# Performance work log

Hardware: AMD Instinct MI355X
Metric: run time of the kernel (lower is better)

The kernel has to match this reference:

```python
import jax, jax.numpy as jnp
import numpy as np

B, Q, K, H, DQ, DK, DV = 16, 128, 512, 128, 128, 128, 128
MASK_VALUE = -1000000.0  # matches d2l.sequence_mask fill value


def setup_inputs() -> dict:
    key = jax.random.key(0)
    ks = jax.random.split(key, 7)
    queries = jax.random.normal(ks[0], (B, Q, DQ), dtype=jnp.float32)
    keys = jax.random.normal(ks[1], (B, K, DK), dtype=jnp.float32)
    values = jax.random.normal(ks[2], (B, K, DV), dtype=jnp.float32)
    valid_lens = jax.random.randint(ks[3], (B,), 1, K + 1, dtype=jnp.int32)
    # Linear params (no bias), scaled like torch default init ~ 1/sqrt(fan_in)
    W_q = jax.random.normal(ks[4], (DQ, H), dtype=jnp.float32) / np.sqrt(DQ)
    W_k = jax.random.normal(ks[5], (DK, H), dtype=jnp.float32) / np.sqrt(DK)
    w_v = jax.random.normal(ks[6], (H,), dtype=jnp.float32) / np.sqrt(H)
    return {"queries": queries, "keys": keys, "values": values,
            "valid_lens": valid_lens, "W_q": W_q, "W_k": W_k, "w_v": w_v}


def reference(queries, keys, values, valid_lens, W_q, W_k, w_v):
    # Project queries and keys: (B,Q,H), (B,K,H)
    q = jnp.einsum("bqd,dh->bqh", queries, W_q)
    k = jnp.einsum("bkd,dh->bkh", keys, W_k)
    # Broadcast add -> tanh -> linear-to-1 score: (B,Q,K)
    features = jnp.tanh(q[:, :, None, :] + k[:, None, :, :])  # (B,Q,K,H)
    scores = jnp.einsum("bqkh,h->bqk", features, w_v)
    # masked softmax over last axis; valid_lens is (B,), broadcast over Q
    mask = jnp.arange(K)[None, None, :] < valid_lens[:, None, None]  # (B,1,K)
    scores = jnp.where(mask, scores, MASK_VALUE)
    attn = jax.nn.softmax(scores, axis=-1)
    # weighted sum over keys: (B,Q,DV)
    return jnp.einsum("bqk,bkv->bqv", attn, values)
```

## Files before the change

kernel.cpp:

```cpp
#include <hip/hip_runtime.h>

#define NB 16
#define NQ 128
#define NK 512
#define NH 128
#define NDV 128

#define KPAD 132

typedef __attribute__((ext_vector_type(8))) short short8;
typedef __attribute__((ext_vector_type(4))) float f32x4;
typedef __attribute__((ext_vector_type(2))) float f32x2;

#define C2LOG2E 2.8853900817779268f
#define LOG2E   1.4426950408889634f

__device__ __forceinline__ short f2bf(float x) {
    unsigned u = __float_as_uint(x);
    unsigned r = (u + 0x7fffu + ((u >> 16) & 1u)) >> 16;
    return (short)r;
}
__device__ __forceinline__ float bf2f(short s) {
    return __uint_as_float(((unsigned)(unsigned short)s) << 16);
}


__global__ __launch_bounds__(256) void wsplit_kernel(
    const float* __restrict__ Wq, const float* __restrict__ Wk,
    const float* __restrict__ wv,
    short* __restrict__ pqh, short* __restrict__ pql,
    short* __restrict__ pkh, short* __restrict__ pkl,
    float* __restrict__ w2)
{
    int blk = blockIdx.x;
    int t   = threadIdx.x;
    if (blk == 0 && t < NH) w2[t] = 2.0f * wv[t];
    int w = blk >> 3, ht = blk & 7;
    int ks = t >> 6, lane = t & 63;
    int m = lane & 15, quad = lane >> 4;
    const float* W = w ? Wk : Wq;
    short* ph = w ? pkh : pqh;
    short* pl = w ? pkl : pql;
    short8 hi, lo;
#pragma unroll
    for (int j = 0; j < 8; ++j) {
        float x = W[(size_t)(ks * 32 + quad * 8 + j) * NH + ht * 16 + m];
        short h = f2bf(x);
        hi[j] = h;
        lo[j] = f2bf(x - bf2f(h));
    }
    size_t o = (size_t)((ht * 4 + ks) * 64 + lane) * 8;
    *(short8*)(ph + o) = hi;
    *(short8*)(pl + o) = lo;
}

__global__ __launch_bounds__(256) void proj_kernel(
    const float* __restrict__ Xq, const float* __restrict__ Xk,
    const short* __restrict__ pqh, const short* __restrict__ pql,
    const short* __restrict__ pkh, const short* __restrict__ pkl,
    float* __restrict__ Eq, float* __restrict__ Ek)
{
    __shared__ float s_x[16 * KPAD];

    int blk = blockIdx.x;
    const float* X; const short* ph; const short* pl; float* Y; int row0;
    if (blk < 128) { X = Xq; ph = pqh; pl = pql; Y = Eq; row0 = blk * 16; }
    else           { X = Xk; ph = pkh; pl = pkl; Y = Ek; row0 = (blk - 128) * 16; }
    int t = threadIdx.x;
    int wave = t >> 6, lane = t & 63;
    int m = lane & 15, quad = lane >> 4;

#pragma unroll
    for (int r = 0; r < 2; ++r) {
        int i = (t + r * 256) * 4;
        int row = i >> 7, col = i & 127;
        *(f32x4*)&s_x[row * KPAD + col] =
            *(const f32x4*)&X[(size_t)(row0 + row) * NH + col];
    }
    __syncthreads();

    short8 AH[4], AL[4];
#pragma unroll
    for (int ks = 0; ks < 4; ++ks) {
        int base = m * KPAD + ks * 32 + quad * 8;
        f32x4 x0 = *(const f32x4*)&s_x[base];
        f32x4 x1 = *(const f32x4*)&s_x[base + 4];
#pragma unroll
        for (int j = 0; j < 4; ++j) {
            short h0 = f2bf(x0[j]);
            AH[ks][j] = h0; AL[ks][j] = f2bf(x0[j] - bf2f(h0));
            short h1 = f2bf(x1[j]);
            AH[ks][j + 4] = h1; AL[ks][j + 4] = f2bf(x1[j] - bf2f(h1));
        }
    }
#pragma unroll
    for (int hi = 0; hi < 2; ++hi) {
        int ht = wave * 2 + hi;
        f32x4 acc = {0.f, 0.f, 0.f, 0.f};
#pragma unroll
        for (int ks = 0; ks < 4; ++ks) {
            size_t o = (size_t)((ht * 4 + ks) * 64 + lane) * 8;
            short8 bh = *(const short8*)(ph + o);
            short8 bl = *(const short8*)(pl + o);
            acc = __builtin_amdgcn_mfma_f32_16x16x32_bf16(AH[ks], bl, acc, 0, 0, 0);
            acc = __builtin_amdgcn_mfma_f32_16x16x32_bf16(AL[ks], bh, acc, 0, 0, 0);
            acc = __builtin_amdgcn_mfma_f32_16x16x32_bf16(AH[ks], bh, acc, 0, 0, 0);
        }
#pragma unroll
        for (int r = 0; r < 4; ++r)
            Y[(size_t)(row0 + quad * 4 + r) * NH + ht * 16 + m] =
                __builtin_amdgcn_exp2f(acc[r] * C2LOG2E);
    }
}

__global__ __launch_bounds__(512) void score_kernel(
    const float* __restrict__ Eqp, const float* __restrict__ Ekp,
    const int* __restrict__ vlen, const float* __restrict__ w2,
    float* __restrict__ P)
{
    __shared__ float s_ek[128 * KPAD];

    int blk = blockIdx.x;
    int b    = blk & 15;
    int rest = blk >> 4;
    int qt = rest & 7, kc = rest >> 3;
    int q0 = qt * 16, k0 = kc * 128;
    int t  = threadIdx.x;

    int nv = vlen[b];
    nv = max(1, min(NK, nv));
    float* Pb = P + ((size_t)b * NQ + q0) * NK;

    if (k0 >= nv) {
        int q = t >> 5, kk = (t & 31) * 4;
        f32x4 z = {0.f, 0.f, 0.f, 0.f};
        *(f32x4*)&Pb[(size_t)q * NK + k0 + kk] = z;
        return;
    }

    for (int i = t; i < 128 * 32; i += 512) {
        int row = i >> 5, c4 = i & 31;
        f32x4 v = *(const f32x4*)&Ekp[((size_t)b * NK + k0 + row) * NH + c4 * 4];
        if (k0 + row >= nv) {
            f32x4 z = {0.f, 0.f, 0.f, 0.f};
            v = z;
        }
        *(f32x4*)&s_ek[row * KPAD + c4 * 4] = v;
    }
    __syncthreads();

    int lane = t & 63, w = t >> 6;
    int wu = __builtin_amdgcn_readfirstlane(w);
    int g = wu & 3, hf = wu >> 2;

    float s2 = w2[lane] + w2[lane + 64];
#pragma unroll
    for (int off = 32; off; off >>= 1) s2 += __shfl_xor(s2, off);
    float wsum = 0.5f * s2;

    const float* ek = &s_ek[(hf * 64 + lane) * KPAD];
    const float* e0 = Eqp + ((size_t)b * NQ + q0 + g * 4 + 0) * NH;
    const float* e1 = Eqp + ((size_t)b * NQ + q0 + g * 4 + 1) * NH;
    const float* e2 = Eqp + ((size_t)b * NQ + q0 + g * 4 + 2) * NH;
    const float* e3 = Eqp + ((size_t)b * NQ + q0 + g * 4 + 3) * NH;

    const f32x2 one2 = {1.0f, 1.0f};
    f32x2 v00 = {0.f, 0.f}, v01 = {0.f, 0.f};
    f32x2 v10 = {0.f, 0.f}, v11 = {0.f, 0.f};
    f32x2 v20 = {0.f, 0.f}, v21 = {0.f, 0.f};
    f32x2 v30 = {0.f, 0.f}, v31 = {0.f, 0.f};

#define PKSTEP(accv, qv, kv, wv)                                        \
    {                                                                   \
        f32x2 x = qv * kv + one2;                                       \
        float R = __builtin_amdgcn_rcpf(x[0] * x[1]);                   \
        f32x2 xs = {x[1], x[0]};                                        \
        accv += wv * (R * xs);                                          \
    }

#pragma unroll
    for (int hh = 0; hh < NH; hh += 8) {
        f32x4 kAv = *(const f32x4*)(ek + hh);
        f32x4 kBv = *(const f32x4*)(ek + hh + 4);
        f32x4 wAv = *(const f32x4*)(w2 + hh);
        f32x4 wBv = *(const f32x4*)(w2 + hh + 4);
        f32x2 kA0 = {kAv[0], kAv[1]}, kA1 = {kAv[2], kAv[3]};
        f32x2 kB0 = {kBv[0], kBv[1]}, kB1 = {kBv[2], kBv[3]};
        f32x2 wA0 = {wAv[0], wAv[1]}, wA1 = {wAv[2], wAv[3]};
        f32x2 wB0 = {wBv[0], wBv[1]}, wB1 = {wBv[2], wBv[3]};
        {
            f32x4 qa = *(const f32x4*)(e0 + hh), qb = *(const f32x4*)(e0 + hh + 4);
            f32x2 qa0 = {qa[0], qa[1]}, qa1 = {qa[2], qa[3]};
            f32x2 qb0 = {qb[0], qb[1]}, qb1 = {qb[2], qb[3]};
            PKSTEP(v00, qa0, kA0, wA0); PKSTEP(v01, qa1, kA1, wA1);
            PKSTEP(v00, qb0, kB0, wB0); PKSTEP(v01, qb1, kB1, wB1);
        }
        {
            f32x4 qa = *(const f32x4*)(e1 + hh), qb = *(const f32x4*)(e1 + hh + 4);
            f32x2 qa0 = {qa[0], qa[1]}, qa1 = {qa[2], qa[3]};
            f32x2 qb0 = {qb[0], qb[1]}, qb1 = {qb[2], qb[3]};
            PKSTEP(v10, qa0, kA0, wA0); PKSTEP(v11, qa1, kA1, wA1);
            PKSTEP(v10, qb0, kB0, wB0); PKSTEP(v11, qb1, kB1, wB1);
        }
        {
            f32x4 qa = *(const f32x4*)(e2 + hh), qb = *(const f32x4*)(e2 + hh + 4);
            f32x2 qa0 = {qa[0], qa[1]}, qa1 = {qa[2], qa[3]};
            f32x2 qb0 = {qb[0], qb[1]}, qb1 = {qb[2], qb[3]};
            PKSTEP(v20, qa0, kA0, wA0); PKSTEP(v21, qa1, kA1, wA1);
            PKSTEP(v20, qb0, kB0, wB0); PKSTEP(v21, qb1, kB1, wB1);
        }
        {
            f32x4 qa = *(const f32x4*)(e3 + hh), qb = *(const f32x4*)(e3 + hh + 4);
            f32x2 qa0 = {qa[0], qa[1]}, qa1 = {qa[2], qa[3]};
            f32x2 qb0 = {qb[0], qb[1]}, qb1 = {qb[2], qb[3]};
            PKSTEP(v30, qa0, kA0, wA0); PKSTEP(v31, qa1, kA1, wA1);
            PKSTEP(v30, qb0, kB0, wB0); PKSTEP(v31, qb1, kB1, wB1);
        }
    }
#undef PKSTEP
    float c0 = (v00[0] + v00[1]) + (v01[0] + v01[1]);
    float c1 = (v10[0] + v10[1]) + (v11[0] + v11[1]);
    float c2 = (v20[0] + v20[1]) + (v21[0] + v21[1]);
    float c3 = (v30[0] + v30[1]) + (v31[0] + v31[1]);
    int kg = k0 + hf * 64 + lane;
    bool valid = kg < nv;
    float p0 = valid ? __builtin_amdgcn_exp2f((wsum - c0) * LOG2E) : 0.f;
    float p1 = valid ? __builtin_amdgcn_exp2f((wsum - c1) * LOG2E) : 0.f;
    float p2 = valid ? __builtin_amdgcn_exp2f((wsum - c2) * LOG2E) : 0.f;
    float p3 = valid ? __builtin_amdgcn_exp2f((wsum - c3) * LOG2E) : 0.f;
    float* Pr = Pb + (size_t)(g * 4) * NK + kg;
    Pr[0 * NK] = p0;
    Pr[1 * NK] = p1;
    Pr[2 * NK] = p2;
    Pr[3 * NK] = p3;
}

__global__ __launch_bounds__(512, 4) void av_kernel(
    const float* __restrict__ P, const float* __restrict__ V,
    const int* __restrict__ vlen, float* __restrict__ out)
{
    __shared__ float s_p[4 * NK];
    __shared__ float s_red[8 * 4 * 128];
    __shared__ float s_rsum[4];

    int blk = blockIdx.x;
    int b = blk & 15, qq = blk >> 4;
    int q0 = qq * 4;
    int t = threadIdx.x;

    int nv = vlen[b];
    nv = max(1, min(NK, nv));

    const f32x4* Pv = (const f32x4*)(P + ((size_t)b * NQ + q0) * NK);
    ((f32x4*)s_p)[t] = Pv[t];
    __syncthreads();

    int lane = t & 63, w = t >> 6;

    if (w < 4) {
        const float* pr = &s_p[w * NK];
        f32x4 s0 = *(const f32x4*)(pr + lane * 8);
        f32x4 s1 = *(const f32x4*)(pr + lane * 8 + 4);
        float s = ((s0[0] + s0[1]) + (s0[2] + s0[3])) +
                  ((s1[0] + s1[1]) + (s1[2] + s1[3]));
#pragma unroll
        for (int off = 32; off; off >>= 1) s += __shfl_xor(s, off);
        if (lane == 0) s_rsum[w] = s;
    }

    int par = lane >> 5;
    int dl  = lane & 31;
    int dv0 = dl * 4;
    const float* Vb = V + (size_t)b * NK * NDV + dv0;
    const float* pa = &s_p[0 * NK];
    const float* pb = &s_p[1 * NK];
    const float* pc = &s_p[2 * NK];
    const float* pd = &s_p[3 * NK];
    f32x4 Oa = {0.f, 0.f, 0.f, 0.f};
    f32x4 Ob = {0.f, 0.f, 0.f, 0.f};
    f32x4 Oc = {0.f, 0.f, 0.f, 0.f};
    f32x4 Od = {0.f, 0.f, 0.f, 0.f};

    int k = w * 8;
    for (; k + 8 <= nv; k += 64) {
        f32x4 pA0 = *(const f32x4*)(pa + k);
        f32x4 pA1 = *(const f32x4*)(pa + k + 4);
        f32x4 pB0 = *(const f32x4*)(pb + k);
        f32x4 pB1 = *(const f32x4*)(pb + k + 4);
        f32x4 pC0 = *(const f32x4*)(pc + k);
        f32x4 pC1 = *(const f32x4*)(pc + k + 4);
        f32x4 pD0 = *(const f32x4*)(pd + k);
        f32x4 pD1 = *(const f32x4*)(pd + k + 4);
        f32x4 v0 = *(const f32x4*)(Vb + (size_t)(k + 0 + par) * NDV);
        f32x4 v1 = *(const f32x4*)(Vb + (size_t)(k + 2 + par) * NDV);
        f32x4 v2 = *(const f32x4*)(Vb + (size_t)(k + 4 + par) * NDV);
        f32x4 v3 = *(const f32x4*)(Vb + (size_t)(k + 6 + par) * NDV);
        float a0 = pA0[par], a1 = pA0[2 + par], a2 = pA1[par], a3 = pA1[2 + par];
        float b0 = pB0[par], b1 = pB0[2 + par], b2 = pB1[par], b3 = pB1[2 + par];
        float c0 = pC0[par], c1 = pC0[2 + par], c2 = pC1[par], c3 = pC1[2 + par];
        float d0 = pD0[par], d1 = pD0[2 + par], d2 = pD1[par], d3 = pD1[2 + par];
#pragma unroll
        for (int j = 0; j < 4; ++j) {
            Oa[j] = fmaf(a0, v0[j], Oa[j]); Ob[j] = fmaf(b0, v0[j], Ob[j]);
            Oc[j] = fmaf(c0, v0[j], Oc[j]); Od[j] = fmaf(d0, v0[j], Od[j]);
            Oa[j] = fmaf(a1, v1[j], Oa[j]); Ob[j] = fmaf(b1, v1[j], Ob[j]);
            Oc[j] = fmaf(c1, v1[j], Oc[j]); Od[j] = fmaf(d1, v1[j], Od[j]);
            Oa[j] = fmaf(a2, v2[j], Oa[j]); Ob[j] = fmaf(b2, v2[j], Ob[j]);
            Oc[j] = fmaf(c2, v2[j], Oc[j]); Od[j] = fmaf(d2, v2[j], Od[j]);
            Oa[j] = fmaf(a3, v3[j], Oa[j]); Ob[j] = fmaf(b3, v3[j], Ob[j]);
            Oc[j] = fmaf(c3, v3[j], Oc[j]); Od[j] = fmaf(d3, v3[j], Od[j]);
        }
    }
    if (k < nv) {
        f32x4 z4 = {0.f, 0.f, 0.f, 0.f};
        f32x4 pA0 = *(const f32x4*)(pa + k);
        f32x4 pA1 = *(const f32x4*)(pa + k + 4);
        f32x4 pB0 = *(const f32x4*)(pb + k);
        f32x4 pB1 = *(const f32x4*)(pb + k + 4);
        f32x4 pC0 = *(const f32x4*)(pc + k);
        f32x4 pC1 = *(const f32x4*)(pc + k + 4);
        f32x4 pD0 = *(const f32x4*)(pd + k);
        f32x4 pD1 = *(const f32x4*)(pd + k + 4);
        f32x4 v0 = *(const f32x4*)(Vb + (size_t)(k + 0 + par) * NDV);
        f32x4 v1 = *(const f32x4*)(Vb + (size_t)(k + 2 + par) * NDV);
        f32x4 v2 = *(const f32x4*)(Vb + (size_t)(k + 4 + par) * NDV);
        f32x4 v3 = *(const f32x4*)(Vb + (size_t)(k + 6 + par) * NDV);
        if (k + 0 + par >= nv) v0 = z4;
        if (k + 2 + par >= nv) v1 = z4;
        if (k + 4 + par >= nv) v2 = z4;
        if (k + 6 + par >= nv) v3 = z4;
        float a0 = pA0[par], a1 = pA0[2 + par], a2 = pA1[par], a3 = pA1[2 + par];
        float b0 = pB0[par], b1 = pB0[2 + par], b2 = pB1[par], b3 = pB1[2 + par];
        float c0 = pC0[par], c1 = pC0[2 + par], c2 = pC1[par], c3 = pC1[2 + par];
        float d0 = pD0[par], d1 = pD0[2 + par], d2 = pD1[par], d3 = pD1[2 + par];
#pragma unroll
        for (int j = 0; j < 4; ++j) {
            Oa[j] = fmaf(a0, v0[j], Oa[j]); Ob[j] = fmaf(b0, v0[j], Ob[j]);
            Oc[j] = fmaf(c0, v0[j], Oc[j]); Od[j] = fmaf(d0, v0[j], Od[j]);
            Oa[j] = fmaf(a1, v1[j], Oa[j]); Ob[j] = fmaf(b1, v1[j], Ob[j]);
            Oc[j] = fmaf(c1, v1[j], Oc[j]); Od[j] = fmaf(d1, v1[j], Od[j]);
            Oa[j] = fmaf(a2, v2[j], Oa[j]); Ob[j] = fmaf(b2, v2[j], Ob[j]);
            Oc[j] = fmaf(c2, v2[j], Oc[j]); Od[j] = fmaf(d2, v2[j], Od[j]);
            Oa[j] = fmaf(a3, v3[j], Oa[j]); Ob[j] = fmaf(b3, v3[j], Ob[j]);
            Oc[j] = fmaf(c3, v3[j], Oc[j]); Od[j] = fmaf(d3, v3[j], Od[j]);
        }
    }
#pragma unroll
    for (int j = 0; j < 4; ++j) {
        Oa[j] += __shfl_xor(Oa[j], 32);
        Ob[j] += __shfl_xor(Ob[j], 32);
        Oc[j] += __shfl_xor(Oc[j], 32);
        Od[j] += __shfl_xor(Od[j], 32);
    }
    float* rb = &s_red[w * 512];
    if (par == 0) {
        *(f32x4*)&rb[0 * 128 + dv0] = Oa;
        *(f32x4*)&rb[1 * 128 + dv0] = Ob;
    } else {
        *(f32x4*)&rb[2 * 128 + dv0] = Oc;
        *(f32x4*)&rb[3 * 128 + dv0] = Od;
    }
    __syncthreads();

    int row = t >> 7, dv = t & 127;
    float s = 0.f;
#pragma unroll
    for (int ww = 0; ww < 8; ++ww) s += s_red[ww * 512 + row * 128 + dv];
    out[((size_t)b * NQ + q0 + row) * NDV + dv] = s * (1.0f / s_rsum[row]);
}

extern "C" void kernel_launch(void* const* d_in, const int* in_sizes, int n_in,
                              void* d_out, int out_size, void* d_ws, size_t ws_size,
                              hipStream_t stream) {
    const float* q  = (const float*)d_in[0];
    const float* ks = (const float*)d_in[1];
    const float* vs = (const float*)d_in[2];
    const int*   vl = (const int*)d_in[3];
    const float* wq = (const float*)d_in[4];
    const float* wk = (const float*)d_in[5];
    const float* wv = (const float*)d_in[6];

    float* Eq = (float*)d_ws;
    float* Ek = Eq + 2048 * 128;
    float* P  = Ek + (size_t)8192 * 128;
    float* w2 = P + (size_t)NB * NQ * NK;
    short* pqh = (short*)(w2 + 128);
    short* pql = pqh + 16384;
    short* pkh = pql + 16384;
    short* pkl = pkh + 16384;

    wsplit_kernel<<<16, 256, 0, stream>>>(wq, wk, wv, pqh, pql, pkh, pkl, w2);
    proj_kernel<<<640, 256, 0, stream>>>(q, ks, pqh, pql, pkh, pkl, Eq, Ek);
    score_kernel<<<512, 512, 0, stream>>>(Eq, Ek, vl, w2, P);
    av_kernel<<<512, 512, 0, stream>>>(P, vs, vl, (float*)d_out);
}
```

Before: 99.23 us.

## Fold weight bf16 split into projection and halve score tile size

Removes the separate weight-split kernel. proj_kernel now loads the fp32 W columns directly and does the hi/lo bf16 split in registers, which saves one launch and a workspace round trip but repeats the conversion in every block. score_kernel now uses 256-thread blocks covering 64 keys, with twice as many blocks and half the shared memory, for finer-grained masking skip and better occupancy. The factor of 2 on w_v moves from a precomputed buffer into the final score arithmetic.

```diff
diff --git a/kernel.cpp b/kernel.cpp
--- a/kernel.cpp
+++ b/kernel.cpp
@@ -25,47 +25,17 @@
 }
 
 
-__global__ __launch_bounds__(256) void wsplit_kernel(
-    const float* __restrict__ Wq, const float* __restrict__ Wk,
-    const float* __restrict__ wv,
-    short* __restrict__ pqh, short* __restrict__ pql,
-    short* __restrict__ pkh, short* __restrict__ pkl,
-    float* __restrict__ w2)
-{
-    int blk = blockIdx.x;
-    int t   = threadIdx.x;
-    if (blk == 0 && t < NH) w2[t] = 2.0f * wv[t];
-    int w = blk >> 3, ht = blk & 7;
-    int ks = t >> 6, lane = t & 63;
-    int m = lane & 15, quad = lane >> 4;
-    const float* W = w ? Wk : Wq;
-    short* ph = w ? pkh : pqh;
-    short* pl = w ? pkl : pql;
-    short8 hi, lo;
-#pragma unroll
-    for (int j = 0; j < 8; ++j) {
-        float x = W[(size_t)(ks * 32 + quad * 8 + j) * NH + ht * 16 + m];
-        short h = f2bf(x);
-        hi[j] = h;
-        lo[j] = f2bf(x - bf2f(h));
-    }
-    size_t o = (size_t)((ht * 4 + ks) * 64 + lane) * 8;
-    *(short8*)(ph + o) = hi;
-    *(short8*)(pl + o) = lo;
-}
-
 __global__ __launch_bounds__(256) void proj_kernel(
     const float* __restrict__ Xq, const float* __restrict__ Xk,
-    const short* __restrict__ pqh, const short* __restrict__ pql,
-    const short* __restrict__ pkh, const short* __restrict__ pkl,
+    const float* __restrict__ Wq, const float* __restrict__ Wk,
     float* __restrict__ Eq, float* __restrict__ Ek)
 {
     __shared__ float s_x[16 * KPAD];
 
     int blk = blockIdx.x;
-    const float* X; const short* ph; const short* pl; float* Y; int row0;
-    if (blk < 128) { X = Xq; ph = pqh; pl = pql; Y = Eq; row0 = blk * 16; }
-    else           { X = Xk; ph = pkh; pl = pkl; Y = Ek; row0 = (blk - 128) * 16; }
+    const float* X; const float* W; float* Y; int row0;
+    if (blk < 128) { X = Xq; W = Wq; Y = Eq; row0 = blk * 16; }
+    else           { X = Xk; W = Wk; Y = Ek; row0 = (blk - 128) * 16; }
     int t = threadIdx.x;
     int wave = t >> 6, lane = t & 63;
     int m = lane & 15, quad = lane >> 4;
@@ -96,12 +66,20 @@
 #pragma unroll
     for (int hi = 0; hi < 2; ++hi) {
         int ht = wave * 2 + hi;
+        const float* Wcol = W + ht * 16 + m;
         f32x4 acc = {0.f, 0.f, 0.f, 0.f};
 #pragma unroll
         for (int ks = 0; ks < 4; ++ks) {
-            size_t o = (size_t)((ht * 4 + ks) * 64 + lane) * 8;
-            short8 bh = *(const short8*)(ph + o);
-            short8 bl = *(const short8*)(pl + o);
+            float wx[8];
+#pragma unroll
+            for (int j = 0; j < 8; ++j)
+                wx[j] = Wcol[(size_t)(ks * 32 + quad * 8 + j) * NH];
+            short8 bh, bl;
+#pragma unroll
+            for (int j = 0; j < 8; ++j) {
+                short h = f2bf(wx[j]);
+                bh[j] = h; bl[j] = f2bf(wx[j] - bf2f(h));
+            }
             acc = __builtin_amdgcn_mfma_f32_16x16x32_bf16(AH[ks], bl, acc, 0, 0, 0);
             acc = __builtin_amdgcn_mfma_f32_16x16x32_bf16(AL[ks], bh, acc, 0, 0, 0);
             acc = __builtin_amdgcn_mfma_f32_16x16x32_bf16(AH[ks], bh, acc, 0, 0, 0);
@@ -113,18 +91,18 @@
     }
 }
 
-__global__ __launch_bounds__(512) void score_kernel(
+__global__ __launch_bounds__(256, 4) void score_kernel(
     const float* __restrict__ Eqp, const float* __restrict__ Ekp,
-    const int* __restrict__ vlen, const float* __restrict__ w2,
+    const int* __restrict__ vlen, const float* __restrict__ wvp,
     float* __restrict__ P)
 {
-    __shared__ float s_ek[128 * KPAD];
+    __shared__ float s_ek[64 * KPAD];
 
     int blk = blockIdx.x;
     int b    = blk & 15;
     int rest = blk >> 4;
     int qt = rest & 7, kc = rest >> 3;
-    int q0 = qt * 16, k0 = kc * 128;
+    int q0 = qt * 16, k0 = kc * 64;
     int t  = threadIdx.x;
 
     int nv = vlen[b];
@@ -132,13 +110,13 @@
     float* Pb = P + ((size_t)b * NQ + q0) * NK;
 
     if (k0 >= nv) {
-        int q = t >> 5, kk = (t & 31) * 4;
+        int q = t >> 4, kk = (t & 15) * 4;
         f32x4 z = {0.f, 0.f, 0.f, 0.f};
         *(f32x4*)&Pb[(size_t)q * NK + k0 + kk] = z;
         return;
     }
 
-    for (int i = t; i < 128 * 32; i += 512) {
+    for (int i = t; i < 64 * 32; i += 256) {
         int row = i >> 5, c4 = i & 31;
         f32x4 v = *(const f32x4*)&Ekp[((size_t)b * NK + k0 + row) * NH + c4 * 4];
         if (k0 + row >= nv) {
@@ -150,15 +128,14 @@
     __syncthreads();
 
     int lane = t & 63, w = t >> 6;
-    int wu = __builtin_amdgcn_readfirstlane(w);
-    int g = wu & 3, hf = wu >> 2;
-
-    float s2 = w2[lane] + w2[lane + 64];
+    int g = __builtin_amdgcn_readfirstlane(w);
+
+    float s2 = wvp[lane] + wvp[lane + 64];
 #pragma unroll
     for (int off = 32; off; off >>= 1) s2 += __shfl_xor(s2, off);
-    float wsum = 0.5f * s2;
-
-    const float* ek = &s_ek[(hf * 64 + lane) * KPAD];
+    float wsum = s2;
+
+    const float* ek = &s_ek[lane * KPAD];
     const float* e0 = Eqp + ((size_t)b * NQ + q0 + g * 4 + 0) * NH;
     const float* e1 = Eqp + ((size_t)b * NQ + q0 + g * 4 + 1) * NH;
     const float* e2 = Eqp + ((size_t)b * NQ + q0 + g * 4 + 2) * NH;
@@ -182,8 +159,8 @@
     for (int hh = 0; hh < NH; hh += 8) {
         f32x4 kAv = *(const f32x4*)(ek + hh);
         f32x4 kBv = *(const f32x4*)(ek + hh + 4);
-        f32x4 wAv = *(const f32x4*)(w2 + hh);
-        f32x4 wBv = *(const f32x4*)(w2 + hh + 4);
+        f32x4 wAv = *(const f32x4*)(wvp + hh);
+        f32x4 wBv = *(const f32x4*)(wvp + hh + 4);
         f32x2 kA0 = {kAv[0], kAv[1]}, kA1 = {kAv[2], kAv[3]};
         f32x2 kB0 = {kBv[0], kBv[1]}, kB1 = {kBv[2], kBv[3]};
         f32x2 wA0 = {wAv[0], wAv[1]}, wA1 = {wAv[2], wAv[3]};
@@ -218,11 +195,11 @@
         }
     }
 #undef PKSTEP
-    float c0 = (v00[0] + v00[1]) + (v01[0] + v01[1]);
-    float c1 = (v10[0] + v10[1]) + (v11[0] + v11[1]);
-    float c2 = (v20[0] + v20[1]) + (v21[0] + v21[1]);
-    float c3 = (v30[0] + v30[1]) + (v31[0] + v31[1]);
-    int kg = k0 + hf * 64 + lane;
+    float c0 = 2.0f * ((v00[0] + v00[1]) + (v01[0] + v01[1]));
+    float c1 = 2.0f * ((v10[0] + v10[1]) + (v11[0] + v11[1]));
+    float c2 = 2.0f * ((v20[0] + v20[1]) + (v21[0] + v21[1]));
+    float c3 = 2.0f * ((v30[0] + v30[1]) + (v31[0] + v31[1]));
+    int kg = k0 + lane;
     bool valid = kg < nv;
     float p0 = valid ? __builtin_amdgcn_exp2f((wsum - c0) * LOG2E) : 0.f;
     float p1 = valid ? __builtin_amdgcn_exp2f((wsum - c1) * LOG2E) : 0.f;
@@ -383,14 +360,8 @@
     float* Eq = (float*)d_ws;
     float* Ek = Eq + 2048 * 128;
     float* P  = Ek + (size_t)8192 * 128;
-    float* w2 = P + (size_t)NB * NQ * NK;
-    short* pqh = (short*)(w2 + 128);
-    short* pql = pqh + 16384;
-    short* pkh = pql + 16384;
-    short* pkl = pkh + 16384;
-
-    wsplit_kernel<<<16, 256, 0, stream>>>(wq, wk, wv, pqh, pql, pkh, pkl, w2);
-    proj_kernel<<<640, 256, 0, stream>>>(q, ks, pqh, pql, pkh, pkl, Eq, Ek);
-    score_kernel<<<512, 512, 0, stream>>>(Eq, Ek, vl, w2, P);
+
+    proj_kernel<<<640, 256, 0, stream>>>(q, ks, wq, wk, Eq, Ek);
+    score_kernel<<<1024, 256, 0, stream>>>(Eq, Ek, vl, wv, P);
     av_kernel<<<512, 512, 0, stream>>>(P, vs, vl, (float*)d_out);
 }
```

New measurement: 99.77 us. Within noise of the previous version (+0.5%).
